# Kernel optimization log

Measured on AMD Instinct MI355X. Metric: run time of the kernel, lower is better.

Reference implementation:

```python
import jax, jax.numpy as jnp
import numpy as np

TOP_K = 10
RANKING_WEIGHT = 0.3
UP_WEIGHT = 1.0
DOWN_WEIGHT = 0.5
NEG = 1e9  # finite stand-in for -inf so softmax/grads stay NaN-free


def setup_inputs() -> dict:
    key = jax.random.key(0)
    k1, k2, k3, k4 = jax.random.split(key, 4)
    B, N = 1024, 5000
    up_logits = jax.random.normal(k1, (B, N), jnp.float32)
    down_logits = jax.random.normal(k2, (B, N), jnp.float32)
    y_true = jax.random.normal(k3, (B, N), jnp.float32) * 0.05  # daily returns
    masks = jax.random.randint(k4, (B, N), 0, 2).astype(jnp.int32)
    return {"up_logits": up_logits, "down_logits": down_logits,
            "y_true": y_true, "masks": masks}


def _bce_with_logits(x, z):
    # softplus(x) - x*z  ==  -[z*log(sig(x)) + (1-z)*log(1-sig(x))]
    return jax.nn.softplus(x) - x * z


def reference(up_logits, down_logits, y_true, masks):
    maskb = masks > 0                                   # [B, N]
    maskf = maskb.astype(up_logits.dtype)
    num_valid = maskf.sum(-1)                           # [B]
    nv_safe = jnp.maximum(num_valid, 1.0)
    k = jnp.minimum(TOP_K, num_valid.astype(jnp.int32))  # [B] min(top_k, num)

    # Descending rank of y_true among valid entries (invalid pushed to bottom).
    y_desc = jnp.where(maskb, y_true, -NEG)
    rank_desc = jnp.argsort(jnp.argsort(-y_desc, axis=-1), axis=-1)  # [B, N]
    up_labels = (rank_desc < k[:, None]).astype(up_logits.dtype)

    # Ascending rank (biggest losers) for down path.
    y_asc = jnp.where(maskb, y_true, NEG)
    rank_asc = jnp.argsort(jnp.argsort(y_asc, axis=-1), axis=-1)
    down_labels = (rank_asc < k[:, None]).astype(down_logits.dtype)

    # Mean BCE over valid entries per row.
    up_loss = jnp.sum(_bce_with_logits(up_logits, up_labels) * maskf, -1) / nv_safe
    down_loss = jnp.sum(_bce_with_logits(down_logits, down_labels) * maskf, -1) / nv_safe

    # Listwise KL: softmax over valid entries; kl_div(log p, q, 'batchmean')
    # with 1D input of size num divides the sum by num.
    logp = jax.nn.log_softmax(jnp.where(maskb, up_logits, -NEG), axis=-1)
    logq = jax.nn.log_softmax(jnp.where(maskb, y_true, -NEG), axis=-1)
    q = jnp.exp(logq)
    kl = jnp.sum(jnp.where(maskb, q * (logq - logp), 0.0), -1) / nv_safe

    batch_loss = UP_WEIGHT * up_loss + DOWN_WEIGHT * down_loss + RANKING_WEIGHT * kl
    batch_loss = jnp.where(num_valid > 0, batch_loss, 0.0)  # skip empty rows
    return jnp.sum(batch_loss) / up_logits.shape[0]
```

## Files before the change

### kernel.cpp

```cpp
#include <hip/hip_runtime.h>
#include <math.h>

#define NCOLS_K 5000
#define BLOCK 256
#define TOPKK 10

__device__ __forceinline__ unsigned mono_f32(float f) {
  unsigned u = __float_as_uint(f);
  return (u & 0x80000000u) ? ~u : (u | 0x80000000u);
}

__device__ __forceinline__ float wave_sum_f(float v) {
#pragma unroll
  for (int o = 1; o < 64; o <<= 1) v += __shfl_xor(v, o);
  return v;
}
__device__ __forceinline__ int wave_sum_i(int v) {
#pragma unroll
  for (int o = 1; o < 64; o <<= 1) v += __shfl_xor(v, o);
  return v;
}
__device__ __forceinline__ unsigned wave_max_u(unsigned v) {
#pragma unroll
  for (int o = 1; o < 64; o <<= 1) {
    unsigned w = __shfl_xor(v, o);
    v = w > v ? w : v;
  }
  return v;
}

extern "C" __global__ __launch_bounds__(BLOCK)
void row_loss_kernel(const float* __restrict__ up, const float* __restrict__ down,
                     const float* __restrict__ yt, const int* __restrict__ masks,
                     float* __restrict__ row_out, int ncols) {
  __shared__ float sy[NCOLS_K];
  __shared__ float red_f[2][4];
  __shared__ int red_i[4];
  __shared__ unsigned swtop[4 * TOPKK];
  __shared__ unsigned swbot[4 * TOPKK];
  __shared__ unsigned s_top[TOPKK];
  __shared__ unsigned s_bot[TOPKK];
  __shared__ float red_acc[3][4];

  const int row = blockIdx.x;
  const int tid = threadIdx.x;
  const int lane = tid & 63;
  const int wv = tid >> 6;
  const long long base = (long long)row * ncols;

  int nv_loc = 0;
  float sq_loc = 0.f, sp_loc = 0.f;
  unsigned td[TOPKK], ta[TOPKK];
#pragma unroll
  for (int j = 0; j < TOPKK; ++j) { td[j] = 0u; ta[j] = 0u; }

  for (int i = tid; i < ncols; i += BLOCK) {
    float y = yt[base + i];
    float u = up[base + i];
    int m = masks[base + i];
    bool valid = m > 0;
    sy[i] = valid ? y : -1e9f;
    if (valid) {
      nv_loc++;
      sq_loc += __expf(y);
      sp_loc += __expf(u);
      unsigned kd = mono_f32(y);
      unsigned ka = ~kd;
      if (kd > td[TOPKK - 1]) {
        td[TOPKK - 1] = kd;
#pragma unroll
        for (int p = TOPKK - 1; p > 0; --p) {
          unsigned a = td[p - 1], b = td[p];
          td[p - 1] = b > a ? b : a;
          td[p]     = b > a ? a : b;
        }
      }
      if (ka > ta[TOPKK - 1]) {
        ta[TOPKK - 1] = ka;
#pragma unroll
        for (int p = TOPKK - 1; p > 0; --p) {
          unsigned a = ta[p - 1], b = ta[p];
          ta[p - 1] = b > a ? b : a;
          ta[p]     = b > a ? a : b;
        }
      }
    }
  }

  nv_loc = wave_sum_i(nv_loc);
  sq_loc = wave_sum_f(sq_loc);
  sp_loc = wave_sum_f(sp_loc);
  if (lane == 0) {
    red_i[wv] = nv_loc;
    red_f[0][wv] = sq_loc;
    red_f[1][wv] = sp_loc;
  }

#pragma unroll 1
  for (int r = 0; r < TOPKK; ++r) {
    unsigned m = wave_max_u(td[0]);
    if (td[0] == m && m != 0u) {
#pragma unroll
      for (int j = 0; j < TOPKK - 1; ++j) td[j] = td[j + 1];
      td[TOPKK - 1] = 0u;
    }
    if (lane == 0) swtop[wv * TOPKK + r] = m;
  }
#pragma unroll 1
  for (int r = 0; r < TOPKK; ++r) {
    unsigned m = wave_max_u(ta[0]);
    if (ta[0] == m && m != 0u) {
#pragma unroll
      for (int j = 0; j < TOPKK - 1; ++j) ta[j] = ta[j + 1];
      ta[TOPKK - 1] = 0u;
    }
    if (lane == 0) swbot[wv * TOPKK + r] = m;
  }
  __syncthreads();

  if (wv == 0) {
    unsigned v = (lane < 4 * TOPKK) ? swtop[lane] : 0u;
#pragma unroll 1
    for (int r = 0; r < TOPKK; ++r) {
      unsigned m = wave_max_u(v);
      if (v == m) v = 0u;
      if (lane == 0) s_top[r] = m;
    }
  } else if (wv == 1) {
    unsigned v = (lane < 4 * TOPKK) ? swbot[lane] : 0u;
#pragma unroll 1
    for (int r = 0; r < TOPKK; ++r) {
      unsigned m = wave_max_u(v);
      if (v == m) v = 0u;
      if (lane == 0) s_bot[r] = m;
    }
  }
  __syncthreads();

  const int nv = red_i[0] + red_i[1] + red_i[2] + red_i[3];
  const float sq = (red_f[0][0] + red_f[0][1]) + (red_f[0][2] + red_f[0][3]);
  const float sp = (red_f[1][0] + red_f[1][1]) + (red_f[1][2] + red_f[1][3]);
  const int k = nv < TOPKK ? nv : TOPKK;
  const unsigned thr_top = (k > 0) ? s_top[k - 1] : 0xFFFFFFFFu;
  const unsigned thr_bot = (k > 0) ? s_bot[k - 1] : 0xFFFFFFFFu;
  const float lsq = __logf(sq);
  const float lsp = __logf(sp);

  float accu = 0.f, accd = 0.f, acck = 0.f;
  for (int i = tid; i < ncols; i += BLOCK) {
    float y = sy[i];
    if (y > -1e8f) {
      float u = up[base + i];
      float d = down[base + i];
      unsigned mo = mono_f32(y);
      float lu = (mo >= thr_top) ? 1.f : 0.f;
      float ld = (~mo >= thr_bot) ? 1.f : 0.f;
      accu += fmaxf(u, 0.f) + __logf(1.f + __expf(-fabsf(u))) - u * lu;
      accd += fmaxf(d, 0.f) + __logf(1.f + __expf(-fabsf(d))) - d * ld;
      float lq = y - lsq;
      acck += __expf(lq) * (lq - (u - lsp));
    }
  }
  accu = wave_sum_f(accu);
  accd = wave_sum_f(accd);
  acck = wave_sum_f(acck);
  if (lane == 0) {
    red_acc[0][wv] = accu;
    red_acc[1][wv] = accd;
    red_acc[2][wv] = acck;
  }
  __syncthreads();
  if (tid == 0) {
    float au = (red_acc[0][0] + red_acc[0][1]) + (red_acc[0][2] + red_acc[0][3]);
    float ad = (red_acc[1][0] + red_acc[1][1]) + (red_acc[1][2] + red_acc[1][3]);
    float ak = (red_acc[2][0] + red_acc[2][1]) + (red_acc[2][2] + red_acc[2][3]);
    float loss = (nv > 0) ? (au + 0.5f * ad + 0.3f * ak) / (float)nv : 0.f;
    row_out[row] = loss;
  }
}

extern "C" __global__ __launch_bounds__(BLOCK)
void final_reduce_kernel(const float* __restrict__ rows, float* __restrict__ out,
                         int nrows) {
  __shared__ float red[4];
  float v = 0.f;
  for (int i = threadIdx.x; i < nrows; i += BLOCK) v += rows[i];
  v = wave_sum_f(v);
  int lane = threadIdx.x & 63, wv = threadIdx.x >> 6;
  if (lane == 0) red[wv] = v;
  __syncthreads();
  if (threadIdx.x == 0)
    out[0] = ((red[0] + red[1]) + (red[2] + red[3])) / (float)nrows;
}

extern "C" void kernel_launch(void* const* d_in, const int* in_sizes, int n_in,
                              void* d_out, int out_size, void* d_ws, size_t ws_size,
                              hipStream_t stream) {
  const float* up_logits   = (const float*)d_in[0];
  const float* down_logits = (const float*)d_in[1];
  const float* y_true      = (const float*)d_in[2];
  const int*   masks       = (const int*)d_in[3];

  const int ncols = NCOLS_K;
  const int nrows = in_sizes[0] / ncols;

  float* rowbuf = (float*)d_ws;

  row_loss_kernel<<<nrows, BLOCK, 0, stream>>>(up_logits, down_logits, y_true,
                                               masks, rowbuf, ncols);
  final_reduce_kernel<<<1, BLOCK, 0, stream>>>(rowbuf, (float*)d_out, nrows);
}
```

Baseline: 143.5 us.

## Single-pass row loss with register caching, float4 loads, algebraic KL, atomic reduce

Each row is now read once with float4 vector loads and held in registers, replacing the shared-memory y buffer and the second global pass over up/down. The KL term is rewritten algebraically as (Σe^y·y − Σe^y·u)/Σe^y − log Σe^y + log Σe^u, and the BCE softplus sums are accumulated in the first pass, so the second pass only sums logits at top-k positions. The final reduce kernel is replaced by a memset plus one atomicAdd per row. The costs are higher register pressure (60 floats cached per thread, with launch bounds asking for 4 blocks), a nondeterministic atomic summation order, and the algebraic KL may lose some precision.

```diff
diff --git a/kernel.cpp b/kernel.cpp
--- a/kernel.cpp
+++ b/kernel.cpp
@@ -1,8 +1,10 @@
 #include <hip/hip_runtime.h>
 #include <math.h>
 
-#define NCOLS_K 5000
+#define NCOLS 5000
+#define NF4   1250
 #define BLOCK 256
+#define NITER 5
 #define TOPKK 10
 
 __device__ __forceinline__ unsigned mono_f32(float f) {
@@ -29,71 +31,95 @@
   return v;
 }
 
-extern "C" __global__ __launch_bounds__(BLOCK)
+__device__ __forceinline__ void insert_desc(unsigned* L, unsigned key) {
+  if (key > L[TOPKK - 1]) {
+    L[TOPKK - 1] = key;
+#pragma unroll
+    for (int p = TOPKK - 1; p > 0; --p) {
+      unsigned a = L[p - 1], b = L[p];
+      L[p - 1] = b > a ? b : a;
+      L[p]     = b > a ? a : b;
+    }
+  }
+}
+
+extern "C" __global__ __launch_bounds__(BLOCK, 4)
 void row_loss_kernel(const float* __restrict__ up, const float* __restrict__ down,
                      const float* __restrict__ yt, const int* __restrict__ masks,
-                     float* __restrict__ row_out, int ncols) {
-  __shared__ float sy[NCOLS_K];
-  __shared__ float red_f[2][4];
+                     float* __restrict__ out, float inv_nrows) {
+  __shared__ float red_f[6][4];
   __shared__ int red_i[4];
   __shared__ unsigned swtop[4 * TOPKK];
   __shared__ unsigned swbot[4 * TOPKK];
-  __shared__ unsigned s_top[TOPKK];
-  __shared__ unsigned s_bot[TOPKK];
-  __shared__ float red_acc[3][4];
+  __shared__ unsigned s_thr[2];
+  __shared__ float red2[2][4];
 
   const int row = blockIdx.x;
   const int tid = threadIdx.x;
   const int lane = tid & 63;
   const int wv = tid >> 6;
-  const long long base = (long long)row * ncols;
-
-  int nv_loc = 0;
-  float sq_loc = 0.f, sp_loc = 0.f;
+  const long long b4 = (long long)row * NF4;
+
+  const float4* up4 = (const float4*)up + b4;
+  const float4* dn4 = (const float4*)down + b4;
+  const float4* yt4 = (const float4*)yt + b4;
+  const int4*   mk4 = (const int4*)masks + b4;
+
+  float ym[NITER][4], uu[NITER][4], dd[NITER][4];
+
+  int nv_l = 0;
+  float sq = 0.f, sp = 0.f, seyy = 0.f, seyu = 0.f, aspu = 0.f, aspd = 0.f;
   unsigned td[TOPKK], ta[TOPKK];
 #pragma unroll
   for (int j = 0; j < TOPKK; ++j) { td[j] = 0u; ta[j] = 0u; }
 
-  for (int i = tid; i < ncols; i += BLOCK) {
-    float y = yt[base + i];
-    float u = up[base + i];
-    int m = masks[base + i];
-    bool valid = m > 0;
-    sy[i] = valid ? y : -1e9f;
-    if (valid) {
-      nv_loc++;
-      sq_loc += __expf(y);
-      sp_loc += __expf(u);
-      unsigned kd = mono_f32(y);
-      unsigned ka = ~kd;
-      if (kd > td[TOPKK - 1]) {
-        td[TOPKK - 1] = kd;
-#pragma unroll
-        for (int p = TOPKK - 1; p > 0; --p) {
-          unsigned a = td[p - 1], b = td[p];
-          td[p - 1] = b > a ? b : a;
-          td[p]     = b > a ? a : b;
-        }
+#pragma unroll
+  for (int j = 0; j < NITER; ++j) {
+    const int f = j * BLOCK + tid;
+    const bool inb = (f < NF4);
+    float4 y4 = make_float4(0.f, 0.f, 0.f, 0.f);
+    float4 u4 = y4, d4 = y4;
+    int4 m4 = make_int4(0, 0, 0, 0);
+    if (inb) { y4 = yt4[f]; u4 = up4[f]; d4 = dn4[f]; m4 = mk4[f]; }
+    const float* yp = (const float*)&y4;
+    const float* upp = (const float*)&u4;
+    const float* dp = (const float*)&d4;
+    const int* mp = (const int*)&m4;
+#pragma unroll
+    for (int c = 0; c < 4; ++c) {
+      const bool valid = mp[c] > 0;
+      const float y = yp[c], u = upp[c], d = dp[c];
+      ym[j][c] = valid ? y : -1e9f;
+      uu[j][c] = u;
+      dd[j][c] = d;
+      if (valid) {
+        nv_l++;
+        const float ey = __expf(y);
+        sq += ey;
+        seyy += ey * y;
+        seyu += ey * u;
+        sp += __expf(u);
+        aspu += fmaxf(u, 0.f) + __logf(1.f + __expf(-fabsf(u)));
+        aspd += fmaxf(d, 0.f) + __logf(1.f + __expf(-fabsf(d)));
+        const unsigned kd = mono_f32(y);
+        insert_desc(td, kd);
+        insert_desc(ta, ~kd);
       }
-      if (ka > ta[TOPKK - 1]) {
-        ta[TOPKK - 1] = ka;
-#pragma unroll
-        for (int p = TOPKK - 1; p > 0; --p) {
-          unsigned a = ta[p - 1], b = ta[p];
-          ta[p - 1] = b > a ? b : a;
-          ta[p]     = b > a ? a : b;
-        }
-      }
-    }
-  }
-
-  nv_loc = wave_sum_i(nv_loc);
-  sq_loc = wave_sum_f(sq_loc);
-  sp_loc = wave_sum_f(sp_loc);
+    }
+  }
+
+  nv_l = wave_sum_i(nv_l);
+  sq = wave_sum_f(sq);
+  sp = wave_sum_f(sp);
+  seyy = wave_sum_f(seyy);
+  seyu = wave_sum_f(seyu);
+  aspu = wave_sum_f(aspu);
+  aspd = wave_sum_f(aspd);
   if (lane == 0) {
-    red_i[wv] = nv_loc;
-    red_f[0][wv] = sq_loc;
-    red_f[1][wv] = sp_loc;
+    red_i[wv] = nv_l;
+    red_f[0][wv] = sq;  red_f[1][wv] = sp;
+    red_f[2][wv] = seyy; red_f[3][wv] = seyu;
+    red_f[4][wv] = aspu; red_f[5][wv] = aspd;
   }
 
 #pragma unroll 1
@@ -118,79 +144,68 @@
   }
   __syncthreads();
 
+  const int nv = red_i[0] + red_i[1] + red_i[2] + red_i[3];
+  const int k = nv < TOPKK ? nv : TOPKK;
+
   if (wv == 0) {
     unsigned v = (lane < 4 * TOPKK) ? swtop[lane] : 0u;
+    unsigned thr = 0xFFFFFFFFu;
 #pragma unroll 1
     for (int r = 0; r < TOPKK; ++r) {
       unsigned m = wave_max_u(v);
       if (v == m) v = 0u;
-      if (lane == 0) s_top[r] = m;
-    }
+      if (r == k - 1) thr = m;
+    }
+    if (lane == 0) s_thr[0] = thr;
   } else if (wv == 1) {
     unsigned v = (lane < 4 * TOPKK) ? swbot[lane] : 0u;
+    unsigned thr = 0xFFFFFFFFu;
 #pragma unroll 1
     for (int r = 0; r < TOPKK; ++r) {
       unsigned m = wave_max_u(v);
       if (v == m) v = 0u;
-      if (lane == 0) s_bot[r] = m;
-    }
+      if (r == k - 1) thr = m;
+    }
+    if (lane == 0) s_thr[1] = thr;
   }
   __syncthreads();
 
-  const int nv = red_i[0] + red_i[1] + red_i[2] + red_i[3];
-  const float sq = (red_f[0][0] + red_f[0][1]) + (red_f[0][2] + red_f[0][3]);
-  const float sp = (red_f[1][0] + red_f[1][1]) + (red_f[1][2] + red_f[1][3]);
-  const int k = nv < TOPKK ? nv : TOPKK;
-  const unsigned thr_top = (k > 0) ? s_top[k - 1] : 0xFFFFFFFFu;
-  const unsigned thr_bot = (k > 0) ? s_bot[k - 1] : 0xFFFFFFFFu;
-  const float lsq = __logf(sq);
-  const float lsp = __logf(sp);
-
-  float accu = 0.f, accd = 0.f, acck = 0.f;
-  for (int i = tid; i < ncols; i += BLOCK) {
-    float y = sy[i];
-    if (y > -1e8f) {
-      float u = up[base + i];
-      float d = down[base + i];
-      unsigned mo = mono_f32(y);
-      float lu = (mo >= thr_top) ? 1.f : 0.f;
-      float ld = (~mo >= thr_bot) ? 1.f : 0.f;
-      accu += fmaxf(u, 0.f) + __logf(1.f + __expf(-fabsf(u))) - u * lu;
-      accd += fmaxf(d, 0.f) + __logf(1.f + __expf(-fabsf(d))) - d * ld;
-      float lq = y - lsq;
-      acck += __expf(lq) * (lq - (u - lsp));
-    }
-  }
-  accu = wave_sum_f(accu);
-  accd = wave_sum_f(accd);
-  acck = wave_sum_f(acck);
-  if (lane == 0) {
-    red_acc[0][wv] = accu;
-    red_acc[1][wv] = accd;
-    red_acc[2][wv] = acck;
-  }
+  const unsigned thr_top = s_thr[0];
+  const unsigned thr_bot = s_thr[1];
+
+  float su = 0.f, sd = 0.f;
+#pragma unroll
+  for (int j = 0; j < NITER; ++j) {
+#pragma unroll
+    for (int c = 0; c < 4; ++c) {
+      const float y = ym[j][c];
+      if (y > -1e8f) {
+        const unsigned mo = mono_f32(y);
+        if (mo >= thr_top) su += uu[j][c];
+        if (~mo >= thr_bot) sd += dd[j][c];
+      }
+    }
+  }
+  su = wave_sum_f(su);
+  sd = wave_sum_f(sd);
+  if (lane == 0) { red2[0][wv] = su; red2[1][wv] = sd; }
   __syncthreads();
-  if (tid == 0) {
-    float au = (red_acc[0][0] + red_acc[0][1]) + (red_acc[0][2] + red_acc[0][3]);
-    float ad = (red_acc[1][0] + red_acc[1][1]) + (red_acc[1][2] + red_acc[1][3]);
-    float ak = (red_acc[2][0] + red_acc[2][1]) + (red_acc[2][2] + red_acc[2][3]);
-    float loss = (nv > 0) ? (au + 0.5f * ad + 0.3f * ak) / (float)nv : 0.f;
-    row_out[row] = loss;
-  }
-}
-
-extern "C" __global__ __launch_bounds__(BLOCK)
-void final_reduce_kernel(const float* __restrict__ rows, float* __restrict__ out,
-                         int nrows) {
-  __shared__ float red[4];
-  float v = 0.f;
-  for (int i = threadIdx.x; i < nrows; i += BLOCK) v += rows[i];
-  v = wave_sum_f(v);
-  int lane = threadIdx.x & 63, wv = threadIdx.x >> 6;
-  if (lane == 0) red[wv] = v;
-  __syncthreads();
-  if (threadIdx.x == 0)
-    out[0] = ((red[0] + red[1]) + (red[2] + red[3])) / (float)nrows;
+
+  if (tid == 0 && nv > 0) {
+    const float SQ = (red_f[0][0] + red_f[0][1]) + (red_f[0][2] + red_f[0][3]);
+    const float SP = (red_f[1][0] + red_f[1][1]) + (red_f[1][2] + red_f[1][3]);
+    const float SYY = (red_f[2][0] + red_f[2][1]) + (red_f[2][2] + red_f[2][3]);
+    const float SYU = (red_f[3][0] + red_f[3][1]) + (red_f[3][2] + red_f[3][3]);
+    const float ASU = (red_f[4][0] + red_f[4][1]) + (red_f[4][2] + red_f[4][3]);
+    const float ASD = (red_f[5][0] + red_f[5][1]) + (red_f[5][2] + red_f[5][3]);
+    const float SU = (red2[0][0] + red2[0][1]) + (red2[0][2] + red2[0][3]);
+    const float SD = (red2[1][0] + red2[1][1]) + (red2[1][2] + red2[1][3]);
+    const float kl = (SYY - SYU) / SQ - __logf(SQ) + __logf(SP);
+    const float up_loss = ASU - SU;
+    const float dn_loss = ASD - SD;
+    const float loss = (up_loss + 0.5f * dn_loss + 0.3f * kl) / (float)nv;
+    atomicAdd(out, loss * inv_nrows);
+  }
 }
 
 extern "C" void kernel_launch(void* const* d_in, const int* in_sizes, int n_in,
@@ -201,12 +216,10 @@
   const float* y_true      = (const float*)d_in[2];
   const int*   masks       = (const int*)d_in[3];
 
-  const int ncols = NCOLS_K;
-  const int nrows = in_sizes[0] / ncols;
-
-  float* rowbuf = (float*)d_ws;
-
+  const int nrows = in_sizes[0] / NCOLS;
+
+  hipMemsetAsync(d_out, 0, sizeof(float) * (size_t)out_size, stream);
   row_loss_kernel<<<nrows, BLOCK, 0, stream>>>(up_logits, down_logits, y_true,
-                                               masks, rowbuf, ncols);
-  final_reduce_kernel<<<1, BLOCK, 0, stream>>>(rowbuf, (float*)d_out, nrows);
-}
+                                               masks, (float*)d_out,
+                                               1.0f / (float)nrows);
+}
```

New measurement: 126.1 us. 1.14x faster.
